# Kernel tuning notes

Hardware: AMD Instinct MI355X
Metric: run time of the kernel (lower is better)

Reference implementation:

```python
import jax, jax.numpy as jnp
import numpy as np

LOG2 = 0.6931471805599453

def ssp(x):
    # ShiftedSoftplus: softplus(x) - log(2)
    return jax.nn.softplus(x) - jnp.asarray(LOG2, x.dtype)

def setup_inputs() -> dict:
    key = jax.random.key(0)
    ks = jax.random.split(key, 12)
    B, N, D, F, R, P = 1, 50000, 128, 128, 20, 1600000
    s = lambda fan_in: 1.0 / np.sqrt(fan_in)
    return {
        "x": jax.random.normal(ks[0], (B, N, D), jnp.float32),
        "f_ij": jax.random.uniform(ks[1], (P, R), jnp.float32),
        "idx_i": jax.random.randint(ks[2], (P,), 0, B * N),
        "idx_j": jax.random.randint(ks[3], (P,), 0, B * N),
        "rcut_ij": jax.random.uniform(ks[4], (P,), jnp.float32),
        "W_in": jax.random.uniform(ks[5], (F, D), jnp.float32, -s(D), s(D)),
        "b_in": jax.random.uniform(ks[6], (F,), jnp.float32, -s(D), s(D)),
        "W_filter": jax.random.uniform(ks[7], (F, R), jnp.float32, -s(R), s(R)),
        "b_filter": jax.random.uniform(ks[8], (F,), jnp.float32, -s(R), s(R)),
        "W_out": jax.random.uniform(ks[9], (D, F), jnp.float32, -s(F), s(F)),
        "b_out": jax.random.uniform(ks[10], (D,), jnp.float32, -s(F), s(F)),
    }

def reference(x, f_ij, idx_i, idx_j, rcut_ij, W_in, b_in, W_filter, b_filter, W_out, b_out):
    B, N, _ = x.shape
    # input_to_feature: Linear(nr_atom_basis -> nr_filters)
    h = jnp.einsum('bnd,fd->bnf', x, W_in) + b_in          # [B,N,F]
    h = h.reshape(B * N, -1)                                # [B*N,F]
    # filter network: Linear(nr_rbf -> nr_filters) + ShiftedSoftplus, scaled by cutoff
    Wij = ssp(jnp.einsum('pr,fr->pf', f_ij, W_filter) + b_filter) * rcut_ij[:, None]  # [P,F]
    # gather -> mul -> scatter_add
    x_ij = h[idx_j] * Wij                                   # [P,F]
    agg = jax.ops.segment_sum(x_ij, idx_i, num_segments=B * N)  # [B*N,F]
    # feature_to_output: Linear(nr_filters -> nr_atom_basis) + ShiftedSoftplus
    out = ssp(jnp.einsum('nf,df->nd', agg, W_out) + b_out)  # [B*N,D]
    return out.reshape(B, N, 128)
```

## Files before the change

### kernel.cpp

```cpp
#include <hip/hip_runtime.h>
#include <hip/hip_bf16.h>

static constexpr float kLog2 = 0.6931471805599453f;

__device__ __forceinline__ float sspf(float x) {
    return fmaxf(x, 0.0f) + __logf(1.0f + __expf(-fabsf(x))) - kLog2;
}

typedef __attribute__((ext_vector_type(8))) _Float16 half8;
typedef __attribute__((ext_vector_type(4))) _Float16 half4v;
typedef __attribute__((ext_vector_type(4))) float float4v;

template <bool ACT, typename OUT>
__device__ __forceinline__ void gemm_mfma_body(const float* __restrict__ A,
                                               const float* __restrict__ B,
                                               const float* __restrict__ bias,
                                               OUT* __restrict__ C, int M,
                                               int blockid) {
    constexpr int LDH = 136;
    __shared__ _Float16 Als[64 * LDH];
    __shared__ _Float16 Bls[128 * LDH];
    const int tid = threadIdx.x;
    const int rowbase = blockid * 64;
#pragma unroll
    for (int j = 0; j < 8; ++j) {
        int idx = j * 256 + tid;
        int r = idx >> 5, c4 = (idx & 31) << 2;
        int rg = rowbase + r;
        rg = rg < M ? rg : (M - 1);
        float4 v = *(const float4*)(A + (size_t)rg * 128 + c4);
        half4v hv = {(_Float16)v.x, (_Float16)v.y, (_Float16)v.z, (_Float16)v.w};
        *(half4v*)&Als[r * LDH + c4] = hv;
    }
#pragma unroll
    for (int j = 0; j < 16; ++j) {
        int idx = j * 256 + tid;
        int r = idx >> 5, c4 = (idx & 31) << 2;
        float4 v = *(const float4*)(B + (size_t)r * 128 + c4);
        half4v hv = {(_Float16)v.x, (_Float16)v.y, (_Float16)v.z, (_Float16)v.w};
        *(half4v*)&Bls[r * LDH + c4] = hv;
    }
    __syncthreads();

    const int wave = tid >> 6, lane = tid & 63;
    const int l15 = lane & 15, q = lane >> 4;
    float4v acc[8];
#pragma unroll
    for (int nt = 0; nt < 8; ++nt) acc[nt] = (float4v){0.f, 0.f, 0.f, 0.f};
    const int am = wave * 16 + l15;
#pragma unroll
    for (int kk = 0; kk < 4; ++kk) {
        half8 af = *(const half8*)&Als[am * LDH + kk * 32 + q * 8];
#pragma unroll
        for (int nt = 0; nt < 8; ++nt) {
            half8 bfv = *(const half8*)&Bls[(nt * 16 + l15) * LDH + kk * 32 + q * 8];
            acc[nt] = __builtin_amdgcn_mfma_f32_16x16x32_f16(af, bfv, acc[nt], 0, 0, 0);
        }
    }
#pragma unroll
    for (int nt = 0; nt < 8; ++nt) {
        int n = nt * 16 + l15;
        float bv = bias[n];
#pragma unroll
        for (int r = 0; r < 4; ++r) {
            int m = rowbase + wave * 16 + q * 4 + r;
            if (m < M) {
                float v = acc[nt][r] + bv;
                if (ACT) v = sspf(v);
                C[(size_t)m * 128 + n] = (OUT)v;
            }
        }
    }
}

__global__ __launch_bounds__(256) void gemm_in_count_kernel(
    const float* __restrict__ A, const float* __restrict__ B,
    const float* __restrict__ bias, _Float16* __restrict__ C, int M,
    const int* __restrict__ idx_i, int* __restrict__ counts, int P,
    int gemm_blocks) {
    if ((int)blockIdx.x < gemm_blocks) {
        gemm_mfma_body<false, _Float16>(A, B, bias, C, M, blockIdx.x);
    } else {
        const int nthr = (gridDim.x - gemm_blocks) * 256;
        for (int p = (blockIdx.x - gemm_blocks) * 256 + threadIdx.x; p < P;
             p += nthr)
            atomicAdd(&counts[idx_i[p]], 1);
    }
}

__global__ __launch_bounds__(256) void gemm_out_kernel(
    const float* __restrict__ A, const float* __restrict__ B,
    const float* __restrict__ bias, float* __restrict__ C, int M) {
    gemm_mfma_body<true, float>(A, B, bias, C, M, blockIdx.x);
}

__global__ __launch_bounds__(256) void alloc_starts_kernel(
    const int* __restrict__ counts, int* __restrict__ starts,
    int* __restrict__ cursor, int* __restrict__ gtot, int N) {
    __shared__ int s[256];
    __shared__ int base;
    const int t = threadIdx.x, g = blockIdx.x * 256 + t;
    const int c = g < N ? counts[g] : 0;
    s[t] = c;
    __syncthreads();
    for (int o = 1; o < 256; o <<= 1) {
        int v = t >= o ? s[t - o] : 0;
        __syncthreads();
        s[t] += v;
        __syncthreads();
    }
    if (t == 255) base = atomicAdd(gtot, s[255]);
    __syncthreads();
    const int excl = base + s[t] - c;
    if (g < N) {
        starts[g] = excl;
        cursor[g] = excl;
    }
}

template <bool EF>
__global__ __launch_bounds__(256) void fill_kernel(
    const int* __restrict__ idx_i, const int* __restrict__ idx_j,
    const float* __restrict__ rcut, const float* __restrict__ f_ij,
    int* __restrict__ cursor, _Float16* __restrict__ ef,
    int2* __restrict__ meta, int* __restrict__ pidx, int P) {
    int p = blockIdx.x * 256 + threadIdx.x;
    if (p >= P) return;
    const int i = idx_i[p];
    const int pos = atomicAdd(&cursor[i], 1);
    meta[pos] = make_int2(idx_j[p] << 7, __float_as_int(rcut[p]));
    if (EF) {
        const float* fr = f_ij + (size_t)p * 20;
        _Float16 hb[24];
#pragma unroll
        for (int r = 0; r < 20; r += 4) {
            float4 v = *(const float4*)(fr + r);
            hb[r] = (_Float16)v.x; hb[r + 1] = (_Float16)v.y;
            hb[r + 2] = (_Float16)v.z; hb[r + 3] = (_Float16)v.w;
        }
        hb[20] = (_Float16)1.0f; hb[21] = (_Float16)0.0f;
        hb[22] = (_Float16)0.0f; hb[23] = (_Float16)0.0f;
        _Float16* dst = ef + (size_t)pos * 24;
        *(half8*)dst = *(half8*)hb;
        *(half8*)(dst + 8) = *(half8*)(hb + 8);
        *(half8*)(dst + 16) = *(half8*)(hb + 16);
    } else {
        pidx[pos] = p;
    }
}

template <bool EF>
__global__ __launch_bounds__(256) void gather_mfma_kernel(
    const _Float16* __restrict__ ef, const int2* __restrict__ meta,
    const int* __restrict__ pidx, const float* __restrict__ f_ij,
    const float* __restrict__ Wf, const float* __restrict__ bf,
    const _Float16* __restrict__ h16, const int* __restrict__ starts,
    const int* __restrict__ counts, float* __restrict__ agg, int N) {
    const int lane = threadIdx.x & 63;
    const int gwave = (blockIdx.x * 256 + threadIdx.x) >> 6;
    const int nwaves = (gridDim.x * 256) >> 6;
    const int l15 = lane & 15, q = lane >> 4;

    half8 wfr[8];
#pragma unroll
    for (int nt = 0; nt < 8; ++nt) {
        const float* wr = Wf + (size_t)(nt * 16 + l15) * 20;
        float v[8];
#pragma unroll
        for (int j = 0; j < 8; ++j) {
            int k = q * 8 + j;
            v[j] = (k < 20) ? wr[k] : ((k == 20) ? bf[nt * 16 + l15] : 0.0f);
        }
        wfr[nt] = (half8){(_Float16)v[0], (_Float16)v[1], (_Float16)v[2],
                          (_Float16)v[3], (_Float16)v[4], (_Float16)v[5],
                          (_Float16)v[6], (_Float16)v[7]};
    }
    const float4v zero = {0.f, 0.f, 0.f, 0.f};

    for (int i = gwave; i < N; i += nwaves) {
        const int s = __builtin_amdgcn_readfirstlane(starts[i]);
        const int cnt = __builtin_amdgcn_readfirstlane(counts[i]);
        const int e = s + cnt;
        float4v acc[8];
#pragma unroll
        for (int nt = 0; nt < 8; ++nt) acc[nt] = zero;

        if (cnt > 0) {
            int pos = min(s + l15, e - 1);
            half8 bf_n = {};
            if (EF) {
                if (q < 3) bf_n = *(const half8*)(ef + (size_t)pos * 24 + q * 8);
            }
            int2 mt_n = meta[pos];
            int p_n = EF ? 0 : pidx[pos];

            for (int c = s; c < e; c += 16) {
                half8 bf_c = bf_n;
                int2 mt_c = mt_n;
                int p_c = p_n;
                if (c + 16 < e) {
                    int np = min(c + 16 + l15, e - 1);
                    if (EF) {
                        if (q < 3) bf_n = *(const half8*)(ef + (size_t)np * 24 + q * 8);
                    } else {
                        p_n = pidx[np];
                    }
                    mt_n = meta[np];
                }
                if (!EF) {
                    const float* fp = f_ij + (size_t)p_c * 20;
                    float b0 = 0.f, b1 = 0.f, b2 = 0.f, b3 = 0.f;
                    float b4 = 0.f, b5 = 0.f, b6 = 0.f, b7 = 0.f;
                    if (q <= 2) {
                        float4 a = *(const float4*)(fp + q * 8);
                        b0 = a.x; b1 = a.y; b2 = a.z; b3 = a.w;
                    }
                    if (q <= 1) {
                        float4 bb = *(const float4*)(fp + q * 8 + 4);
                        b4 = bb.x; b5 = bb.y; b6 = bb.z; b7 = bb.w;
                    }
                    if (q == 2) b4 = 1.0f;
                    bf_c = (half8){(_Float16)b0, (_Float16)b1, (_Float16)b2,
                                   (_Float16)b3, (_Float16)b4, (_Float16)b5,
                                   (_Float16)b6, (_Float16)b7};
                }
                const int jb = mt_c.x;
                const float rc = (c + l15 < e) ? __int_as_float(mt_c.y) : 0.0f;
                half4v hv[8];
#pragma unroll
                for (int nt = 0; nt < 8; ++nt)
                    hv[nt] = *(const half4v*)(h16 + jb + nt * 16 + q * 4);
#pragma unroll
                for (int nt = 0; nt < 8; ++nt) {
                    float4v d = __builtin_amdgcn_mfma_f32_16x16x32_f16(
                        wfr[nt], bf_c, zero, 0, 0, 0);
#pragma unroll
                    for (int r = 0; r < 4; ++r) {
                        float w = sspf(d[r]) * rc;
                        acc[nt][r] = fmaf(w, (float)hv[nt][r], acc[nt][r]);
                    }
                }
            }
        }
#pragma unroll
        for (int m = 1; m <= 8; m <<= 1)
#pragma unroll
            for (int nt = 0; nt < 8; ++nt)
#pragma unroll
                for (int r = 0; r < 4; ++r)
                    acc[nt][r] += __shfl_xor(acc[nt][r], m, 64);
        if (l15 == 0) {
#pragma unroll
            for (int nt = 0; nt < 8; ++nt) {
                float4 o = {acc[nt][0], acc[nt][1], acc[nt][2], acc[nt][3]};
                *(float4*)(agg + (size_t)i * 128 + nt * 16 + q * 4) = o;
            }
        }
    }
}

extern "C" void kernel_launch(void* const* d_in, const int* in_sizes, int n_in,
                              void* d_out, int out_size, void* d_ws, size_t ws_size,
                              hipStream_t stream) {
    const float* x     = (const float*)d_in[0];
    const float* f_ij  = (const float*)d_in[1];
    const int*   idx_i = (const int*)d_in[2];
    const int*   idx_j = (const int*)d_in[3];
    const float* rcut  = (const float*)d_in[4];
    const float* W_in  = (const float*)d_in[5];
    const float* b_in  = (const float*)d_in[6];
    const float* W_f   = (const float*)d_in[7];
    const float* b_f   = (const float*)d_in[8];
    const float* W_out = (const float*)d_in[9];
    const float* b_out = (const float*)d_in[10];

    const int N = in_sizes[0] / 128;
    const int P = in_sizes[2];

    char* ws = (char*)d_ws;
    size_t off = 0;
    auto alloc = [&](size_t bytes) {
        void* ptr = ws + off;
        off += (bytes + 15) & ~(size_t)15;
        return ptr;
    };
    int* counts  = (int*)alloc((size_t)N * 4 + 16);
    int* gtot    = counts + N;
    int* starts  = (int*)alloc((size_t)N * 4);
    int* cursor  = (int*)alloc((size_t)N * 4);
    _Float16* h16 = (_Float16*)alloc((size_t)N * 128 * 2);
    int2* meta   = (int2*)alloc((size_t)P * 8);
    size_t base_need = off;
    const bool use_ef = (base_need + (size_t)P * 24 * 2 + 64) <= ws_size;
    _Float16* ef = nullptr;
    int* pidx = nullptr;
    if (use_ef) ef = (_Float16*)alloc((size_t)P * 24 * 2 + 64);
    else        pidx = (int*)alloc((size_t)P * 4);

    float* agg = (float*)d_out;

    const int mblocks = (N + 63) / 64;
    const int cblocks = 768;
    const int NB = (N + 255) / 256;

    hipMemsetAsync(counts, 0, (size_t)N * 4 + 16, stream);
    gemm_in_count_kernel<<<mblocks + cblocks, 256, 0, stream>>>(
        x, W_in, b_in, h16, N, idx_i, counts, P, mblocks);
    alloc_starts_kernel<<<NB, 256, 0, stream>>>(counts, starts, cursor, gtot, N);
    if (use_ef) {
        fill_kernel<true><<<(P + 255) / 256, 256, 0, stream>>>(
            idx_i, idx_j, rcut, f_ij, cursor, ef, meta, pidx, P);
        gather_mfma_kernel<true><<<2048, 256, 0, stream>>>(
            ef, meta, pidx, f_ij, W_f, b_f, h16, starts, counts, agg, N);
    } else {
        fill_kernel<false><<<(P + 255) / 256, 256, 0, stream>>>(
            idx_i, idx_j, rcut, f_ij, cursor, ef, meta, pidx, P);
        gather_mfma_kernel<false><<<2048, 256, 0, stream>>>(
            ef, meta, pidx, f_ij, W_f, b_f, h16, starts, counts, agg, N);
    }
    gemm_out_kernel<<<mblocks, 256, 0, stream>>>(agg, W_out, b_out, (float*)d_out, N);
}
```

Measured before the change: 632.1 us.

## Split gather filters across wave pairs and prefetch h rows one chunk ahead

```diff
diff --git a/kernel.cpp b/kernel.cpp
--- a/kernel.cpp
+++ b/kernel.cpp
@@ -150,7 +150,7 @@
 }
 
 template <bool EF>
-__global__ __launch_bounds__(256) void gather_mfma_kernel(
+__global__ __launch_bounds__(256, 4) void gather_mfma_kernel(
     const _Float16* __restrict__ ef, const int2* __restrict__ meta,
     const int* __restrict__ pidx, const float* __restrict__ f_ij,
     const float* __restrict__ Wf, const float* __restrict__ bf,
@@ -160,52 +160,83 @@
     const int gwave = (blockIdx.x * 256 + threadIdx.x) >> 6;
     const int nwaves = (gridDim.x * 256) >> 6;
     const int l15 = lane & 15, q = lane >> 4;
-
-    half8 wfr[8];
-#pragma unroll
-    for (int nt = 0; nt < 8; ++nt) {
-        const float* wr = Wf + (size_t)(nt * 16 + l15) * 20;
+    const int fh = gwave & 1;
+    const int fbase = fh * 64;
+
+    half8 wfr[4];
+#pragma unroll
+    for (int t = 0; t < 4; ++t) {
+        const int n = fbase + t * 16 + l15;
+        const float* wr = Wf + (size_t)n * 20;
         float v[8];
 #pragma unroll
         for (int j = 0; j < 8; ++j) {
             int k = q * 8 + j;
-            v[j] = (k < 20) ? wr[k] : ((k == 20) ? bf[nt * 16 + l15] : 0.0f);
-        }
-        wfr[nt] = (half8){(_Float16)v[0], (_Float16)v[1], (_Float16)v[2],
-                          (_Float16)v[3], (_Float16)v[4], (_Float16)v[5],
-                          (_Float16)v[6], (_Float16)v[7]};
+            v[j] = (k < 20) ? wr[k] : ((k == 20) ? bf[n] : 0.0f);
+        }
+        wfr[t] = (half8){(_Float16)v[0], (_Float16)v[1], (_Float16)v[2],
+                         (_Float16)v[3], (_Float16)v[4], (_Float16)v[5],
+                         (_Float16)v[6], (_Float16)v[7]};
     }
     const float4v zero = {0.f, 0.f, 0.f, 0.f};
-
-    for (int i = gwave; i < N; i += nwaves) {
+    const _Float16* hbase = h16 + fbase + q * 4;
+
+    for (int u = gwave; u < 2 * N; u += nwaves) {
+        const int i = u >> 1;
         const int s = __builtin_amdgcn_readfirstlane(starts[i]);
         const int cnt = __builtin_amdgcn_readfirstlane(counts[i]);
         const int e = s + cnt;
-        float4v acc[8];
-#pragma unroll
-        for (int nt = 0; nt < 8; ++nt) acc[nt] = zero;
+        float4v acc[4];
+#pragma unroll
+        for (int t = 0; t < 4; ++t) acc[t] = zero;
 
         if (cnt > 0) {
-            int pos = min(s + l15, e - 1);
-            half8 bf_n = {};
+            int pos0 = min(s + l15, e - 1);
+            int2 mt_c = meta[pos0];
+            half8 bf_c = {};
+            int p_c = 0;
             if (EF) {
-                if (q < 3) bf_n = *(const half8*)(ef + (size_t)pos * 24 + q * 8);
-            }
-            int2 mt_n = meta[pos];
-            int p_n = EF ? 0 : pidx[pos];
+                if (q < 3) bf_c = *(const half8*)(ef + (size_t)pos0 * 24 + q * 8);
+            } else {
+                p_c = pidx[pos0];
+            }
+            int2 mt_n = mt_c;
+            half8 bf_n = bf_c;
+            int p_n = p_c;
+            if (s + 16 < e) {
+                int pos1 = min(s + 16 + l15, e - 1);
+                mt_n = meta[pos1];
+                if (EF) {
+                    if (q < 3) bf_n = *(const half8*)(ef + (size_t)pos1 * 24 + q * 8);
+                } else {
+                    p_n = pidx[pos1];
+                }
+            }
+            half4v hv_c[4];
+            {
+                const _Float16* hp = hbase + mt_c.x;
+#pragma unroll
+                for (int t = 0; t < 4; ++t) hv_c[t] = *(const half4v*)(hp + t * 16);
+            }
 
             for (int c = s; c < e; c += 16) {
-                half8 bf_c = bf_n;
-                int2 mt_c = mt_n;
-                int p_c = p_n;
+                half4v hv_n[4];
                 if (c + 16 < e) {
-                    int np = min(c + 16 + l15, e - 1);
+                    const _Float16* hp = hbase + mt_n.x;
+#pragma unroll
+                    for (int t = 0; t < 4; ++t) hv_n[t] = *(const half4v*)(hp + t * 16);
+                }
+                int2 mt_n2 = mt_n;
+                half8 bf_n2 = bf_n;
+                int p_n2 = p_n;
+                if (c + 32 < e) {
+                    int pos2 = min(c + 32 + l15, e - 1);
+                    mt_n2 = meta[pos2];
                     if (EF) {
-                        if (q < 3) bf_n = *(const half8*)(ef + (size_t)np * 24 + q * 8);
+                        if (q < 3) bf_n2 = *(const half8*)(ef + (size_t)pos2 * 24 + q * 8);
                     } else {
-                        p_n = pidx[np];
+                        p_n2 = pidx[pos2];
                     }
-                    mt_n = meta[np];
                 }
                 if (!EF) {
                     const float* fp = f_ij + (size_t)p_c * 20;
@@ -224,36 +255,36 @@
                                    (_Float16)b3, (_Float16)b4, (_Float16)b5,
                                    (_Float16)b6, (_Float16)b7};
                 }
-                const int jb = mt_c.x;
                 const float rc = (c + l15 < e) ? __int_as_float(mt_c.y) : 0.0f;
-                half4v hv[8];
-#pragma unroll
-                for (int nt = 0; nt < 8; ++nt)
-                    hv[nt] = *(const half4v*)(h16 + jb + nt * 16 + q * 4);
-#pragma unroll
-                for (int nt = 0; nt < 8; ++nt) {
+#pragma unroll
+                for (int t = 0; t < 4; ++t) {
                     float4v d = __builtin_amdgcn_mfma_f32_16x16x32_f16(
-                        wfr[nt], bf_c, zero, 0, 0, 0);
+                        wfr[t], bf_c, zero, 0, 0, 0);
 #pragma unroll
                     for (int r = 0; r < 4; ++r) {
                         float w = sspf(d[r]) * rc;
-                        acc[nt][r] = fmaf(w, (float)hv[nt][r], acc[nt][r]);
+                        acc[t][r] = fmaf(w, (float)hv_c[t][r], acc[t][r]);
                     }
                 }
+                mt_c = mt_n; mt_n = mt_n2;
+                bf_c = bf_n; bf_n = bf_n2;
+                p_c = p_n;   p_n = p_n2;
+#pragma unroll
+                for (int t = 0; t < 4; ++t) hv_c[t] = hv_n[t];
             }
         }
 #pragma unroll
         for (int m = 1; m <= 8; m <<= 1)
 #pragma unroll
-            for (int nt = 0; nt < 8; ++nt)
+            for (int t = 0; t < 4; ++t)
 #pragma unroll
                 for (int r = 0; r < 4; ++r)
-                    acc[nt][r] += __shfl_xor(acc[nt][r], m, 64);
+                    acc[t][r] += __shfl_xor(acc[t][r], m, 64);
         if (l15 == 0) {
 #pragma unroll
-            for (int nt = 0; nt < 8; ++nt) {
-                float4 o = {acc[nt][0], acc[nt][1], acc[nt][2], acc[nt][3]};
-                *(float4*)(agg + (size_t)i * 128 + nt * 16 + q * 4) = o;
+            for (int t = 0; t < 4; ++t) {
+                float4 o = {acc[t][0], acc[t][1], acc[t][2], acc[t][3]};
+                *(float4*)(agg + (size_t)i * 128 + fbase + t * 16 + q * 4) = o;
             }
         }
     }
@@ -310,12 +341,12 @@
     if (use_ef) {
         fill_kernel<true><<<(P + 255) / 256, 256, 0, stream>>>(
             idx_i, idx_j, rcut, f_ij, cursor, ef, meta, pidx, P);
-        gather_mfma_kernel<true><<<2048, 256, 0, stream>>>(
+        gather_mfma_kernel<true><<<4096, 256, 0, stream>>>(
             ef, meta, pidx, f_ij, W_f, b_f, h16, starts, counts, agg, N);
     } else {
         fill_kernel<false><<<(P + 255) / 256, 256, 0, stream>>>(
             idx_i, idx_j, rcut, f_ij, cursor, ef, meta, pidx, P);
-        gather_mfma_kernel<false><<<2048, 256, 0, stream>>>(
+        gather_mfma_kernel<false><<<4096, 256, 0, stream>>>(
             ef, meta, pidx, f_ij, W_f, b_f, h16, starts, counts, agg, N);
     }
     gemm_out_kernel<<<mblocks, 256, 0, stream>>>(agg, W_out, b_out, (float*)d_out, N);
```

Result: no change. 627.3 us (-0.8%).
